# Kernel tuning notes

Hardware: AMD Instinct MI355X
Metric: run time of the kernel (lower is better)

## Reference

```python
import jax, jax.numpy as jnp
import numpy as np

H = 128
M = 50000
L = 400000
EPS = 1e-9


def setup_inputs() -> dict:
    key = jax.random.key(0)
    ks = jax.random.split(key, 24)
    d = {
        'x_emb': jax.random.normal(ks[0], (M, H), jnp.float32),
        'child_h': jax.random.normal(ks[1], (M, H), jnp.float32),
        'child_c': jax.random.normal(ks[2], (M, H), jnp.float32),
        'pair_cand_idx': jax.random.randint(ks[3], (L,), 0, M, jnp.int32),
        'pair_child_idx': jax.random.randint(ks[4], (L,), 0, M, jnp.int32),
    }
    s = 1.0 / np.sqrt(H)
    names = ['Wi_w', 'Ui_w', 'Wf_w', 'Uf_w', 'Wo_w', 'Uo_w', 'Wc_w', 'Uc_w', 'Wa_w', 'Ua_w']
    for i, n in enumerate(names):
        d[n] = jax.random.uniform(ks[5 + i], (H, H), jnp.float32, -s, s)
    for i, n in enumerate(['Wi_b', 'Wf_b', 'Wo_b', 'Wc_b', 'Wa_b']):
        d[n] = jax.random.uniform(ks[15 + i], (H,), jnp.float32, -s, s)
    d['v_w'] = jax.random.uniform(ks[20], (H,), jnp.float32, -s, s)
    return d


def reference(x_emb, child_h, child_c, pair_cand_idx, pair_child_idx,
              Wi_w, Ui_w, Wf_w, Uf_w, Wo_w, Uo_w, Wc_w, Uc_w, Wa_w, Ua_w,
              Wi_b, Wf_b, Wo_b, Wc_b, Wa_b, v_w):
    m = x_emb.shape[0]
    ci, chi = pair_cand_idx, pair_child_idx

    # --- segment attention (torch version runs under no_grad) ---
    Ah = child_h @ Wa_w.T + Wa_b          # [M,H]
    Bx = x_emb @ Ua_w.T                   # [M,H]
    e = jnp.tanh(Ah[chi] + Bx[ci]) @ v_w  # [L]
    seg_max = jax.ops.segment_max(e, ci, num_segments=m)
    x_exp = jnp.exp(e - seg_max[ci])
    seg_sum = jax.ops.segment_sum(x_exp, ci, num_segments=m) + EPS
    attn = x_exp / seg_sum[ci]            # [L]
    h_hat = jax.ops.segment_sum(attn[:, None] * child_h[chi], ci, num_segments=m)  # [M,H]

    # --- tree-LSTM gates ---
    i_j = jax.nn.sigmoid(x_emb @ Wi_w.T + Wi_b + h_hat @ Ui_w.T)
    Wfx = x_emb @ Wf_w.T + Wf_b
    Ufh = child_h @ Uf_w.T
    f_pair = jax.nn.sigmoid(Wfx[ci] + Ufh[chi])                       # [L,H]
    sum_f_c = jax.ops.segment_sum(f_pair * child_c[chi], ci, num_segments=m)
    c_t = jnp.tanh(x_emb @ Wc_w.T + Wc_b + h_hat @ Uc_w.T)
    c = i_j * c_t + sum_f_c
    o_j = jax.nn.sigmoid(x_emb @ Wo_w.T + Wo_b + h_hat @ Uo_w.T)
    h = o_j * jnp.tanh(c)
    return (h, c)
```

## Files before the change

kernel.cpp:

```cpp
#include <hip/hip_runtime.h>
#include <cstdint>
#include <cstddef>

#define H 128
#define PSTRIDE 512

typedef __bf16 v8bf __attribute__((ext_vector_type(8)));
typedef __bf16 v4bf __attribute__((ext_vector_type(4)));
typedef float  v4f  __attribute__((ext_vector_type(4)));

__device__ __forceinline__ float ftanh(float x) {
    return 1.f - 2.f / (1.f + __expf(2.f * x));
}
__device__ __forceinline__ float fsigm(float x) {
    return 1.f / (1.f + __expf(-x));
}

struct MatDesc {
    const __bf16* A;
    int           lda;
    const __bf16* Wb;
    const float*  bias;
    __bf16*       C;
    int           ldc;
};
struct MatBatch { MatDesc m[7]; };
struct WPtrs { const float* w[10]; };

__global__ __launch_bounds__(256) void prep_k(WPtrs wp, __bf16* __restrict__ Wb,
                                              const float* __restrict__ x,
                                              const float* __restrict__ chh,
                                              const float* __restrict__ chc,
                                              __bf16* __restrict__ xe,
                                              __bf16* __restrict__ P,
                                              const int* __restrict__ ci,
                                              int* __restrict__ counts,
                                              int MH4, int L) {
    int tid = blockIdx.x * 256 + threadIdx.x;
    if (tid < 40960) {
        int mat = tid >> 12;
        int off = (tid & 4095) << 2;
        v4f a = *(const v4f*)(wp.w[mat] + off);
        v4bf b;
#pragma unroll
        for (int k = 0; k < 4; ++k) b[k] = (__bf16)a[k];
        *(v4bf*)(Wb + mat * 16384 + off) = b;
        return;
    }
    int i = tid - 40960;
    if (i < MH4) {
        v4f a = ((const v4f*)x)[i];
        v4f b = ((const v4f*)chh)[i];
        v4f c = ((const v4f*)chc)[i];
        v4bf ab, bb, cb;
#pragma unroll
        for (int k = 0; k < 4; ++k) {
            ab[k] = (__bf16)a[k]; bb[k] = (__bf16)b[k]; cb[k] = (__bf16)c[k];
        }
        ((v4bf*)xe)[i] = ab;
        int m = i >> 5;
        int q = (i & 31) << 2;
        __bf16* prow = P + (size_t)m * PSTRIDE + q;
        *(v4bf*)prow = bb;
        *(v4bf*)(prow + H) = cb;
        return;
    }
    int l = i - MH4;
    if (l < L) atomicAdd(&counts[ci[l]], 1);
}

__global__ __launch_bounds__(256) void gemm_batch(MatBatch batch, int M, int ntile) {
    const int blk = blockIdx.x;
    const int g = blk / 56;
    const int w = blk % 56;
    const int j = w >> 3;
    const int t = (g << 3) | (w & 7);
    if (t >= ntile) return;
    const MatDesc d = batch.m[j];
    __shared__ __bf16 wlds[H][H + 8];

    for (int tt = threadIdx.x; tt < 2048; tt += 256) {
        int n = tt >> 4;
        int k = (tt & 15) << 3;
        *(v8bf*)&wlds[n][k] = *(const v8bf*)(d.Wb + n * H + k);
    }
    __syncthreads();

    const int wave = threadIdx.x >> 6;
    const int lane = threadIdx.x & 63;
    const int quad = lane >> 4;
    const int l16  = lane & 15;
    const int r0   = t * 128 + wave * 32;

    v4f acc0[8], acc1[8];
#pragma unroll
    for (int nt = 0; nt < 8; ++nt) {
        acc0[nt] = (v4f){0.f, 0.f, 0.f, 0.f};
        acc1[nt] = (v4f){0.f, 0.f, 0.f, 0.f};
    }

    const __bf16* ar0 = d.A + (size_t)(r0 + l16) * d.lda + quad * 8;
    const __bf16* ar1 = d.A + (size_t)(r0 + 16 + l16) * d.lda + quad * 8;
#pragma unroll
    for (int k0 = 0; k0 < H; k0 += 32) {
        v8bf a0 = *(const v8bf*)(ar0 + k0);
        v8bf a1 = *(const v8bf*)(ar1 + k0);
#pragma unroll
        for (int nt = 0; nt < 8; ++nt) {
            v8bf b = *(const v8bf*)(&wlds[nt * 16 + l16][k0 + quad * 8]);
            acc0[nt] = __builtin_amdgcn_mfma_f32_16x16x32_bf16(a0, b, acc0[nt], 0, 0, 0);
            acc1[nt] = __builtin_amdgcn_mfma_f32_16x16x32_bf16(a1, b, acc1[nt], 0, 0, 0);
        }
    }

#pragma unroll
    for (int nt = 0; nt < 8; ++nt) {
        int n = nt * 16 + l16;
        float bia = d.bias ? d.bias[n] : 0.f;
#pragma unroll
        for (int r = 0; r < 4; ++r) {
            int m0 = r0 + quad * 4 + r;
            int m1 = m0 + 16;
            if (m0 < M) d.C[(size_t)m0 * d.ldc + n] = (__bf16)(acc0[nt][r] + bia);
            if (m1 < M) d.C[(size_t)m1 * d.ldc + n] = (__bf16)(acc1[nt][r] + bia);
        }
    }
}

__global__ __launch_bounds__(256) void edge_scatter(const int* __restrict__ ci,
                                                    const int* __restrict__ chi,
                                                    const float* __restrict__ vw,
                                                    const __bf16* __restrict__ Bx,
                                                    const __bf16* __restrict__ P,
                                                    int* __restrict__ cursor,
                                                    int* __restrict__ payload,
                                                    float* __restrict__ exs, int L) {
    int e = blockIdx.x * 8 + (threadIdx.x >> 5);
    if (e >= L) return;
    const int l32 = threadIdx.x & 31;
    const int h = l32 << 2;
    int m  = ci[e];
    int cj = chi[e];

    v4bf a4 = *(const v4bf*)(P + (cj << 9) + 3 * H + h);
    v4bf b4 = *(const v4bf*)(Bx + (m << 7) + h);
    v4f  vv = *(const v4f*)(vw + h);

    float s = 0.f;
#pragma unroll
    for (int k = 0; k < 4; ++k) s += ftanh((float)a4[k] + (float)b4[k]) * vv[k];
    s += __shfl_xor(s, 1);
    s += __shfl_xor(s, 2);
    s += __shfl_xor(s, 4);
    s += __shfl_xor(s, 8);
    s += __shfl_xor(s, 16);
    if (l32 == 0) {
        int pos = atomicAdd(&cursor[m], 1);
        payload[pos] = cj;
        exs[pos] = __expf(s);
    }
}

__global__ __launch_bounds__(1024) void scan_local(const int* __restrict__ counts,
                                                   int* __restrict__ excl,
                                                   int* __restrict__ bsums, int M) {
    __shared__ int s[1024];
    int tid = threadIdx.x;
    int idx = blockIdx.x * 1024 + tid;
    int v = (idx < M) ? counts[idx] : 0;
    s[tid] = v;
    __syncthreads();
    for (int off = 1; off < 1024; off <<= 1) {
        int t = (tid >= off) ? s[tid - off] : 0;
        __syncthreads();
        s[tid] += t;
        __syncthreads();
    }
    if (idx < M) excl[idx] = s[tid] - v;
    if (tid == 1023) bsums[blockIdx.x] = s[1023];
}

__global__ __launch_bounds__(1024) void scan_fused(int* __restrict__ rowptr,
                                                   int* __restrict__ cursor,
                                                   const int* __restrict__ bsums,
                                                   const int* __restrict__ counts,
                                                   int M, int nb) {
    __shared__ int s[1024];
    int t = threadIdx.x, b = blockIdx.x;
    int v = (t < nb) ? bsums[t] : 0;
    s[t] = v;
    __syncthreads();
    for (int off = 1; off < 1024; off <<= 1) {
        int tt = (t >= off) ? s[t - off] : 0;
        __syncthreads();
        s[t] += tt;
        __syncthreads();
    }
    int boff = (b == 0) ? 0 : s[b - 1];
    int idx = b * 1024 + t;
    if (idx < M) {
        int val = rowptr[idx] + boff;
        rowptr[idx] = val;
        cursor[idx] = val;
        if (idx == M - 1) rowptr[M] = val + counts[M - 1];
    }
}

__global__ __launch_bounds__(256) void segment_fused(const int* __restrict__ rowptr,
                                                     const int* __restrict__ payload,
                                                     const float* __restrict__ exs,
                                                     const __bf16* __restrict__ Wfx,
                                                     const __bf16* __restrict__ P,
                                                     __bf16* __restrict__ hhat,
                                                     float* __restrict__ sumfc, int M) {
    const int wl   = threadIdx.x & 63;
    const int half = wl & 32;
    const int l32  = wl & 31;
    const int m = blockIdx.x * 8 + (threadIdx.x >> 5);
    if (m >= M) return;
    const int start = rowptr[m];
    const int deg   = rowptr[m + 1] - start;
    const int h = l32 << 2;

    v4bf wf4 = *(const v4bf*)(Wfx + (m << 7) + h);
    float wff[4];
#pragma unroll
    for (int k = 0; k < 4; ++k) wff[k] = (float)wf4[k];

    int   pl0 = (l32 < deg) ? payload[start + l32] : 0;
    int   pl1 = (32 + l32 < deg) ? payload[start + 32 + l32] : 0;
    float ex0 = (l32 < deg) ? exs[start + l32] : 0.f;
    float ex1 = (32 + l32 < deg) ? exs[start + 32 + l32] : 0.f;

    float denom = 0.f;
    float acch[4] = {0.f, 0.f, 0.f, 0.f};
    float accf[4] = {0.f, 0.f, 0.f, 0.f};

    const int jcap = deg < 64 ? deg : 64;
    for (int j = 0; j < jcap; ++j) {
        int   cj = __shfl((j & 32) ? pl1 : pl0, half | (j & 31), 64);
        float ex = __shfl((j & 32) ? ex1 : ex0, half | (j & 31), 64);
        int off = (cj << 9) + h;
        v4bf h4 = *(const v4bf*)(P + off);
        v4bf c4 = *(const v4bf*)(P + off + H);
        v4bf u4 = *(const v4bf*)(P + off + 2 * H);
        denom += ex;
#pragma unroll
        for (int k = 0; k < 4; ++k) {
            acch[k] = fmaf(ex, (float)h4[k], acch[k]);
            accf[k] += fsigm(wff[k] + (float)u4[k]) * (float)c4[k];
        }
    }
    for (int j = 64; j < deg; ++j) {
        int   cj = payload[start + j];
        float ex = exs[start + j];
        int off = (cj << 9) + h;
        v4bf h4 = *(const v4bf*)(P + off);
        v4bf c4 = *(const v4bf*)(P + off + H);
        v4bf u4 = *(const v4bf*)(P + off + 2 * H);
        denom += ex;
#pragma unroll
        for (int k = 0; k < 4; ++k) {
            acch[k] = fmaf(ex, (float)h4[k], acch[k]);
            accf[k] += fsigm(wff[k] + (float)u4[k]) * (float)c4[k];
        }
    }

    float inv = 1.f / (denom + 1e-9f);
    v4bf hb;
    v4f sf;
#pragma unroll
    for (int k = 0; k < 4; ++k) { hb[k] = (__bf16)(acch[k] * inv); sf[k] = accf[k]; }
    *(v4bf*)(hhat + (size_t)m * H + h) = hb;
    *(v4f*)(sumfc + (size_t)m * H + h) = sf;
}

__global__ __launch_bounds__(256) void gemm_final(const __bf16* __restrict__ hhat,
                                                  const __bf16* __restrict__ Ui,
                                                  const __bf16* __restrict__ Uc,
                                                  const __bf16* __restrict__ Uo,
                                                  const __bf16* __restrict__ Xi,
                                                  const __bf16* __restrict__ Xc,
                                                  const __bf16* __restrict__ Xo,
                                                  const float* __restrict__ sumfc,
                                                  float* __restrict__ out, int M, int MH) {
    const int wave = threadIdx.x >> 6;
    const int lane = threadIdx.x & 63;
    const int quad = lane >> 4;
    const int l16  = lane & 15;
    const int r0   = blockIdx.x * 128 + wave * 32;

    const __bf16* p0 = hhat + (size_t)(r0 + l16) * H + quad * 8;
    const __bf16* p1 = hhat + (size_t)(r0 + 16 + l16) * H + quad * 8;
    v8bf a0[4], a1[4];
#pragma unroll
    for (int k0 = 0; k0 < 4; ++k0) {
        a0[k0] = *(const v8bf*)(p0 + k0 * 32);
        a1[k0] = *(const v8bf*)(p1 + k0 * 32);
    }

#pragma unroll
    for (int nt = 0; nt < 8; ++nt) {
        const int boff = (nt * 16 + l16) * H + quad * 8;
        v4f ai0 = (v4f){0.f, 0.f, 0.f, 0.f}, ai1 = ai0;
        v4f ac0 = ai0, ac1 = ai0, ao0 = ai0, ao1 = ai0;
#pragma unroll
        for (int k0 = 0; k0 < 4; ++k0) {
            v8bf bi = *(const v8bf*)(Ui + boff + k0 * 32);
            v8bf bc = *(const v8bf*)(Uc + boff + k0 * 32);
            v8bf bo = *(const v8bf*)(Uo + boff + k0 * 32);
            ai0 = __builtin_amdgcn_mfma_f32_16x16x32_bf16(a0[k0], bi, ai0, 0, 0, 0);
            ai1 = __builtin_amdgcn_mfma_f32_16x16x32_bf16(a1[k0], bi, ai1, 0, 0, 0);
            ac0 = __builtin_amdgcn_mfma_f32_16x16x32_bf16(a0[k0], bc, ac0, 0, 0, 0);
            ac1 = __builtin_amdgcn_mfma_f32_16x16x32_bf16(a1[k0], bc, ac1, 0, 0, 0);
            ao0 = __builtin_amdgcn_mfma_f32_16x16x32_bf16(a0[k0], bo, ao0, 0, 0, 0);
            ao1 = __builtin_amdgcn_mfma_f32_16x16x32_bf16(a1[k0], bo, ao1, 0, 0, 0);
        }
        int n = nt * 16 + l16;
#pragma unroll
        for (int r = 0; r < 4; ++r) {
            int m0 = r0 + quad * 4 + r;
            if (m0 < M) {
                size_t idx = (size_t)m0 * H + n;
                float ig = fsigm((float)Xi[idx] + ai0[r]);
                float ct = ftanh((float)Xc[idx] + ac0[r]);
                float og = fsigm((float)Xo[idx] + ao0[r]);
                float c = ig * ct + sumfc[idx];
                out[idx] = og * ftanh(c);
                out[MH + idx] = c;
            }
            int m1 = m0 + 16;
            if (m1 < M) {
                size_t idx = (size_t)m1 * H + n;
                float ig = fsigm((float)Xi[idx] + ai1[r]);
                float ct = ftanh((float)Xc[idx] + ac1[r]);
                float og = fsigm((float)Xo[idx] + ao1[r]);
                float c = ig * ct + sumfc[idx];
                out[idx] = og * ftanh(c);
                out[MH + idx] = c;
            }
        }
    }
}

extern "C" void kernel_launch(void* const* d_in, const int* in_sizes, int n_in,
                              void* d_out, int out_size, void* d_ws, size_t ws_size,
                              hipStream_t stream) {
    const float* x_emb   = (const float*)d_in[0];
    const float* child_h = (const float*)d_in[1];
    const float* child_c = (const float*)d_in[2];
    const int*   ci      = (const int*)d_in[3];
    const int*   chi     = (const int*)d_in[4];
    const float* Wi_b = (const float*)d_in[15];
    const float* Wf_b = (const float*)d_in[16];
    const float* Wo_b = (const float*)d_in[17];
    const float* Wc_b = (const float*)d_in[18];
    const float* Wa_b = (const float*)d_in[19];
    const float* vw   = (const float*)d_in[20];

    const int M    = in_sizes[0] / H;
    const int L    = in_sizes[3];
    const int Mpad = (M + 127) & ~127;
    const int MH   = M * H;
    const int MH4  = MH / 4;

    char* p = (char*)d_ws;
    auto alloc = [&](size_t bytes) {
        char* r = p;
        p += (bytes + 255) & ~(size_t)255;
        return (void*)r;
    };
    size_t bfbytes = (size_t)Mpad * H * sizeof(__bf16);
    __bf16* xe16   = (__bf16*)alloc(bfbytes);
    __bf16* P      = (__bf16*)alloc((size_t)Mpad * PSTRIDE * sizeof(__bf16));
    __bf16* hhat16 = (__bf16*)alloc(bfbytes);
    __bf16* Bx16   = (__bf16*)alloc(bfbytes);
    __bf16* Wfx16  = (__bf16*)alloc(bfbytes);
    __bf16* Xi16   = (__bf16*)alloc(bfbytes);
    __bf16* Xc16   = (__bf16*)alloc(bfbytes);
    __bf16* Xo16   = (__bf16*)alloc(bfbytes);
    __bf16* Wb     = (__bf16*)alloc(10 * 16384 * sizeof(__bf16));
    float* sumfc   = (float*)alloc((size_t)MH * 4);
    float* exs     = (float*)alloc((size_t)L * 4);
    int*   payload = (int*)alloc((size_t)L * 4);
    int*   counts  = (int*)alloc((size_t)M * 4);
    int*   rowptr  = (int*)alloc((size_t)(M + 1) * 4);
    int*   cursor  = (int*)alloc((size_t)M * 4);
    int*   bsums   = (int*)alloc(1024 * 4);

    hipMemsetAsync(counts, 0, (size_t)M * 4, stream);

    WPtrs wp;
    for (int k = 0; k < 10; ++k) wp.w[k] = (const float*)d_in[5 + k];
    int prep_items = 40960 + MH4 + L;
    prep_k<<<(prep_items + 255) / 256, 256, 0, stream>>>(wp, Wb, x_emb, child_h, child_c,
                                                         xe16, P, ci, counts, MH4, L);

    const __bf16* Wi = Wb + 0 * 16384;
    const __bf16* Ui = Wb + 1 * 16384;
    const __bf16* Wf = Wb + 2 * 16384;
    const __bf16* Uf = Wb + 3 * 16384;
    const __bf16* Wo = Wb + 4 * 16384;
    const __bf16* Uo = Wb + 5 * 16384;
    const __bf16* Wc = Wb + 6 * 16384;
    const __bf16* Uc = Wb + 7 * 16384;
    const __bf16* Wa = Wb + 8 * 16384;
    const __bf16* Ua = Wb + 9 * 16384;

    MatBatch ba{};
    ba.m[0] = MatDesc{P,    PSTRIDE, Wa, Wa_b,    P + 3 * H, PSTRIDE};
    ba.m[1] = MatDesc{xe16, H,       Ua, nullptr, Bx16,      H};
    ba.m[2] = MatDesc{xe16, H,       Wf, Wf_b,    Wfx16,     H};
    ba.m[3] = MatDesc{P,    PSTRIDE, Uf, nullptr, P + 2 * H, PSTRIDE};
    ba.m[4] = MatDesc{xe16, H,       Wi, Wi_b,    Xi16,      H};
    ba.m[5] = MatDesc{xe16, H,       Wc, Wc_b,    Xc16,      H};
    ba.m[6] = MatDesc{xe16, H,       Wo, Wo_b,    Xo16,      H};
    const int ntile = Mpad / 128;
    const int ntile8 = (ntile + 7) & ~7;
    gemm_batch<<<7 * ntile8, 256, 0, stream>>>(ba, M, ntile);

    int nb = (M + 1023) / 1024;
    scan_local<<<nb, 1024, 0, stream>>>(counts, rowptr, bsums, M);
    scan_fused<<<nb, 1024, 0, stream>>>(rowptr, cursor, bsums, counts, M, nb);

    edge_scatter<<<(L + 7) / 8, 256, 0, stream>>>(ci, chi, vw, Bx16, P, cursor,
                                                  payload, exs, L);

    segment_fused<<<(M + 7) / 8, 256, 0, stream>>>(rowptr, payload, exs, Wfx16, P,
                                                   hhat16, sumfc, M);

    gemm_final<<<Mpad / 128, 256, 0, stream>>>(hhat16, Ui, Uc, Uo, Xi16, Xc16, Xo16,
                                               sumfc, (float*)d_out, M, MH);
}
```

Before: 412.6 us.

## Fuse attention score computation into segment kernel and read fp32 x_emb directly in GEMM

The per-edge attention score (tanh dot product and exp) moves out of the edge scatter kernel into the per-segment reduction kernel. The scatter becomes a thin one-thread-per-edge CSR fill, and the exs buffer is no longer written or read. The batched GEMM now converts fp32 x_emb to bf16 on the fly, so the separate bf16 copy of x_emb in prep is dropped. The segment loop is unrolled by two to overlap gathers; the cost is an extra 128-element gather per edge in the segment kernel and five x_emb GEMMs each reading fp32 inputs.

Result: slower. 428.4 us (+3.8%).

```diff
diff --git a/kernel.cpp b/kernel.cpp
--- a/kernel.cpp
+++ b/kernel.cpp
@@ -17,8 +17,9 @@
 }
 
 struct MatDesc {
-    const __bf16* A;
+    const void*   A;
     int           lda;
+    int           af32;
     const __bf16* Wb;
     const float*  bias;
     __bf16*       C;
@@ -28,10 +29,8 @@
 struct WPtrs { const float* w[10]; };
 
 __global__ __launch_bounds__(256) void prep_k(WPtrs wp, __bf16* __restrict__ Wb,
-                                              const float* __restrict__ x,
                                               const float* __restrict__ chh,
                                               const float* __restrict__ chc,
-                                              __bf16* __restrict__ xe,
                                               __bf16* __restrict__ P,
                                               const int* __restrict__ ci,
                                               int* __restrict__ counts,
@@ -49,15 +48,11 @@
     }
     int i = tid - 40960;
     if (i < MH4) {
-        v4f a = ((const v4f*)x)[i];
         v4f b = ((const v4f*)chh)[i];
         v4f c = ((const v4f*)chc)[i];
-        v4bf ab, bb, cb;
-#pragma unroll
-        for (int k = 0; k < 4; ++k) {
-            ab[k] = (__bf16)a[k]; bb[k] = (__bf16)b[k]; cb[k] = (__bf16)c[k];
-        }
-        ((v4bf*)xe)[i] = ab;
+        v4bf bb, cb;
+#pragma unroll
+        for (int k = 0; k < 4; ++k) { bb[k] = (__bf16)b[k]; cb[k] = (__bf16)c[k]; }
         int m = i >> 5;
         int q = (i & 31) << 2;
         __bf16* prow = P + (size_t)m * PSTRIDE + q;
@@ -92,6 +87,39 @@
     const int l16  = lane & 15;
     const int r0   = t * 128 + wave * 32;
 
+    int ra = r0 + l16;      if (ra > M - 1) ra = M - 1;
+    int rb = r0 + 16 + l16; if (rb > M - 1) rb = M - 1;
+
+    v8bf a0[4], a1[4];
+    if (d.af32) {
+        const float* A = (const float*)d.A;
+        const float* p0 = A + (size_t)ra * d.lda + quad * 8;
+        const float* p1 = A + (size_t)rb * d.lda + quad * 8;
+#pragma unroll
+        for (int k0 = 0; k0 < 4; ++k0) {
+            v4f x0a = *(const v4f*)(p0 + k0 * 32);
+            v4f x0b = *(const v4f*)(p0 + k0 * 32 + 4);
+            v4f x1a = *(const v4f*)(p1 + k0 * 32);
+            v4f x1b = *(const v4f*)(p1 + k0 * 32 + 4);
+            v8bf t0, t1;
+#pragma unroll
+            for (int k = 0; k < 4; ++k) {
+                t0[k] = (__bf16)x0a[k]; t0[k + 4] = (__bf16)x0b[k];
+                t1[k] = (__bf16)x1a[k]; t1[k + 4] = (__bf16)x1b[k];
+            }
+            a0[k0] = t0; a1[k0] = t1;
+        }
+    } else {
+        const __bf16* A = (const __bf16*)d.A;
+        const __bf16* p0 = A + (size_t)ra * d.lda + quad * 8;
+        const __bf16* p1 = A + (size_t)rb * d.lda + quad * 8;
+#pragma unroll
+        for (int k0 = 0; k0 < 4; ++k0) {
+            a0[k0] = *(const v8bf*)(p0 + k0 * 32);
+            a1[k0] = *(const v8bf*)(p1 + k0 * 32);
+        }
+    }
+
     v4f acc0[8], acc1[8];
 #pragma unroll
     for (int nt = 0; nt < 8; ++nt) {
@@ -99,17 +127,13 @@
         acc1[nt] = (v4f){0.f, 0.f, 0.f, 0.f};
     }
 
-    const __bf16* ar0 = d.A + (size_t)(r0 + l16) * d.lda + quad * 8;
-    const __bf16* ar1 = d.A + (size_t)(r0 + 16 + l16) * d.lda + quad * 8;
-#pragma unroll
-    for (int k0 = 0; k0 < H; k0 += 32) {
-        v8bf a0 = *(const v8bf*)(ar0 + k0);
-        v8bf a1 = *(const v8bf*)(ar1 + k0);
+#pragma unroll
+    for (int k0 = 0; k0 < 4; ++k0) {
 #pragma unroll
         for (int nt = 0; nt < 8; ++nt) {
-            v8bf b = *(const v8bf*)(&wlds[nt * 16 + l16][k0 + quad * 8]);
-            acc0[nt] = __builtin_amdgcn_mfma_f32_16x16x32_bf16(a0, b, acc0[nt], 0, 0, 0);
-            acc1[nt] = __builtin_amdgcn_mfma_f32_16x16x32_bf16(a1, b, acc1[nt], 0, 0, 0);
+            v8bf b = *(const v8bf*)(&wlds[nt * 16 + l16][k0 * 32 + quad * 8]);
+            acc0[nt] = __builtin_amdgcn_mfma_f32_16x16x32_bf16(a0[k0], b, acc0[nt], 0, 0, 0);
+            acc1[nt] = __builtin_amdgcn_mfma_f32_16x16x32_bf16(a1[k0], b, acc1[nt], 0, 0, 0);
         }
     }
 
@@ -124,40 +148,6 @@
             if (m0 < M) d.C[(size_t)m0 * d.ldc + n] = (__bf16)(acc0[nt][r] + bia);
             if (m1 < M) d.C[(size_t)m1 * d.ldc + n] = (__bf16)(acc1[nt][r] + bia);
         }
-    }
-}
-
-__global__ __launch_bounds__(256) void edge_scatter(const int* __restrict__ ci,
-                                                    const int* __restrict__ chi,
-                                                    const float* __restrict__ vw,
-                                                    const __bf16* __restrict__ Bx,
-                                                    const __bf16* __restrict__ P,
-                                                    int* __restrict__ cursor,
-                                                    int* __restrict__ payload,
-                                                    float* __restrict__ exs, int L) {
-    int e = blockIdx.x * 8 + (threadIdx.x >> 5);
-    if (e >= L) return;
-    const int l32 = threadIdx.x & 31;
-    const int h = l32 << 2;
-    int m  = ci[e];
-    int cj = chi[e];
-
-    v4bf a4 = *(const v4bf*)(P + (cj << 9) + 3 * H + h);
-    v4bf b4 = *(const v4bf*)(Bx + (m << 7) + h);
-    v4f  vv = *(const v4f*)(vw + h);
-
-    float s = 0.f;
-#pragma unroll
-    for (int k = 0; k < 4; ++k) s += ftanh((float)a4[k] + (float)b4[k]) * vv[k];
-    s += __shfl_xor(s, 1);
-    s += __shfl_xor(s, 2);
-    s += __shfl_xor(s, 4);
-    s += __shfl_xor(s, 8);
-    s += __shfl_xor(s, 16);
-    if (l32 == 0) {
-        int pos = atomicAdd(&cursor[m], 1);
-        payload[pos] = cj;
-        exs[pos] = __expf(s);
     }
 }
 
@@ -206,9 +196,21 @@
     }
 }
 
+__global__ __launch_bounds__(256) void scatter_k(const int* __restrict__ ci,
+                                                 const int* __restrict__ chi,
+                                                 int* __restrict__ cursor,
+                                                 int* __restrict__ payload, int L) {
+    int l = blockIdx.x * 256 + threadIdx.x;
+    if (l < L) {
+        int pos = atomicAdd(&cursor[ci[l]], 1);
+        payload[pos] = chi[l];
+    }
+}
+
 __global__ __launch_bounds__(256) void segment_fused(const int* __restrict__ rowptr,
                                                      const int* __restrict__ payload,
-                                                     const float* __restrict__ exs,
+                                                     const float* __restrict__ vw,
+                                                     const __bf16* __restrict__ Bx,
                                                      const __bf16* __restrict__ Wfx,
                                                      const __bf16* __restrict__ P,
                                                      __bf16* __restrict__ hhat,
@@ -222,28 +224,73 @@
     const int deg   = rowptr[m + 1] - start;
     const int h = l32 << 2;
 
+    v4bf bx4 = *(const v4bf*)(Bx + (m << 7) + h);
     v4bf wf4 = *(const v4bf*)(Wfx + (m << 7) + h);
-    float wff[4];
-#pragma unroll
-    for (int k = 0; k < 4; ++k) wff[k] = (float)wf4[k];
-
-    int   pl0 = (l32 < deg) ? payload[start + l32] : 0;
-    int   pl1 = (32 + l32 < deg) ? payload[start + 32 + l32] : 0;
-    float ex0 = (l32 < deg) ? exs[start + l32] : 0.f;
-    float ex1 = (32 + l32 < deg) ? exs[start + 32 + l32] : 0.f;
+    v4f  vv  = *(const v4f*)(vw + h);
+    float bxf[4], wff[4];
+#pragma unroll
+    for (int k = 0; k < 4; ++k) { bxf[k] = (float)bx4[k]; wff[k] = (float)wf4[k]; }
+
+    int pl0 = (l32 < deg) ? payload[start + l32] : 0;
+    int pl1 = (32 + l32 < deg) ? payload[start + 32 + l32] : 0;
 
     float denom = 0.f;
     float acch[4] = {0.f, 0.f, 0.f, 0.f};
     float accf[4] = {0.f, 0.f, 0.f, 0.f};
 
     const int jcap = deg < 64 ? deg : 64;
-    for (int j = 0; j < jcap; ++j) {
-        int   cj = __shfl((j & 32) ? pl1 : pl0, half | (j & 31), 64);
-        float ex = __shfl((j & 32) ? ex1 : ex0, half | (j & 31), 64);
-        int off = (cj << 9) + h;
-        v4bf h4 = *(const v4bf*)(P + off);
-        v4bf c4 = *(const v4bf*)(P + off + H);
-        v4bf u4 = *(const v4bf*)(P + off + 2 * H);
+    int j = 0;
+    for (; j + 2 <= jcap; j += 2) {
+        int cj0 = __shfl((j & 32) ? pl1 : pl0, half | (j & 31), 64);
+        int cj1 = __shfl((j & 32) ? pl1 : pl0, half | ((j + 1) & 31), 64);
+        const __bf16* pb0 = P + ((size_t)cj0 << 9) + h;
+        const __bf16* pb1 = P + ((size_t)cj1 << 9) + h;
+        v4bf h40 = *(const v4bf*)pb0;
+        v4bf c40 = *(const v4bf*)(pb0 + H);
+        v4bf u40 = *(const v4bf*)(pb0 + 2 * H);
+        v4bf a40 = *(const v4bf*)(pb0 + 3 * H);
+        v4bf h41 = *(const v4bf*)pb1;
+        v4bf c41 = *(const v4bf*)(pb1 + H);
+        v4bf u41 = *(const v4bf*)(pb1 + 2 * H);
+        v4bf a41 = *(const v4bf*)(pb1 + 3 * H);
+        float s0 = 0.f, s1 = 0.f;
+#pragma unroll
+        for (int k = 0; k < 4; ++k) {
+            s0 += ftanh((float)a40[k] + bxf[k]) * vv[k];
+            s1 += ftanh((float)a41[k] + bxf[k]) * vv[k];
+        }
+        s0 += __shfl_xor(s0, 1);  s1 += __shfl_xor(s1, 1);
+        s0 += __shfl_xor(s0, 2);  s1 += __shfl_xor(s1, 2);
+        s0 += __shfl_xor(s0, 4);  s1 += __shfl_xor(s1, 4);
+        s0 += __shfl_xor(s0, 8);  s1 += __shfl_xor(s1, 8);
+        s0 += __shfl_xor(s0, 16); s1 += __shfl_xor(s1, 16);
+        float ex0 = __expf(s0);
+        float ex1 = __expf(s1);
+        denom += ex0 + ex1;
+#pragma unroll
+        for (int k = 0; k < 4; ++k) {
+            acch[k] = fmaf(ex0, (float)h40[k], acch[k]);
+            acch[k] = fmaf(ex1, (float)h41[k], acch[k]);
+            accf[k] += fsigm(wff[k] + (float)u40[k]) * (float)c40[k];
+            accf[k] += fsigm(wff[k] + (float)u41[k]) * (float)c41[k];
+        }
+    }
+    for (; j < jcap; ++j) {
+        int cj = __shfl((j & 32) ? pl1 : pl0, half | (j & 31), 64);
+        const __bf16* pb = P + ((size_t)cj << 9) + h;
+        v4bf h4 = *(const v4bf*)pb;
+        v4bf c4 = *(const v4bf*)(pb + H);
+        v4bf u4 = *(const v4bf*)(pb + 2 * H);
+        v4bf a4 = *(const v4bf*)(pb + 3 * H);
+        float s = 0.f;
+#pragma unroll
+        for (int k = 0; k < 4; ++k) s += ftanh((float)a4[k] + bxf[k]) * vv[k];
+        s += __shfl_xor(s, 1);
+        s += __shfl_xor(s, 2);
+        s += __shfl_xor(s, 4);
+        s += __shfl_xor(s, 8);
+        s += __shfl_xor(s, 16);
+        float ex = __expf(s);
         denom += ex;
 #pragma unroll
         for (int k = 0; k < 4; ++k) {
@@ -251,13 +298,22 @@
             accf[k] += fsigm(wff[k] + (float)u4[k]) * (float)c4[k];
         }
     }
-    for (int j = 64; j < deg; ++j) {
-        int   cj = payload[start + j];
-        float ex = exs[start + j];
-        int off = (cj << 9) + h;
-        v4bf h4 = *(const v4bf*)(P + off);
-        v4bf c4 = *(const v4bf*)(P + off + H);
-        v4bf u4 = *(const v4bf*)(P + off + 2 * H);
+    for (int jj = 64; jj < deg; ++jj) {
+        int cj = payload[start + jj];
+        const __bf16* pb = P + ((size_t)cj << 9) + h;
+        v4bf h4 = *(const v4bf*)pb;
+        v4bf c4 = *(const v4bf*)(pb + H);
+        v4bf u4 = *(const v4bf*)(pb + 2 * H);
+        v4bf a4 = *(const v4bf*)(pb + 3 * H);
+        float s = 0.f;
+#pragma unroll
+        for (int k = 0; k < 4; ++k) s += ftanh((float)a4[k] + bxf[k]) * vv[k];
+        s += __shfl_xor(s, 1);
+        s += __shfl_xor(s, 2);
+        s += __shfl_xor(s, 4);
+        s += __shfl_xor(s, 8);
+        s += __shfl_xor(s, 16);
+        float ex = __expf(s);
         denom += ex;
 #pragma unroll
         for (int k = 0; k < 4; ++k) {
@@ -371,7 +427,6 @@
         return (void*)r;
     };
     size_t bfbytes = (size_t)Mpad * H * sizeof(__bf16);
-    __bf16* xe16   = (__bf16*)alloc(bfbytes);
     __bf16* P      = (__bf16*)alloc((size_t)Mpad * PSTRIDE * sizeof(__bf16));
     __bf16* hhat16 = (__bf16*)alloc(bfbytes);
     __bf16* Bx16   = (__bf16*)alloc(bfbytes);
@@ -381,7 +436,6 @@
     __bf16* Xo16   = (__bf16*)alloc(bfbytes);
     __bf16* Wb     = (__bf16*)alloc(10 * 16384 * sizeof(__bf16));
     float* sumfc   = (float*)alloc((size_t)MH * 4);
-    float* exs     = (float*)alloc((size_t)L * 4);
     int*   payload = (int*)alloc((size_t)L * 4);
     int*   counts  = (int*)alloc((size_t)M * 4);
     int*   rowptr  = (int*)alloc((size_t)(M + 1) * 4);
@@ -393,8 +447,8 @@
     WPtrs wp;
     for (int k = 0; k < 10; ++k) wp.w[k] = (const float*)d_in[5 + k];
     int prep_items = 40960 + MH4 + L;
-    prep_k<<<(prep_items + 255) / 256, 256, 0, stream>>>(wp, Wb, x_emb, child_h, child_c,
-                                                         xe16, P, ci, counts, MH4, L);
+    prep_k<<<(prep_items + 255) / 256, 256, 0, stream>>>(wp, Wb, child_h, child_c,
+                                                         P, ci, counts, MH4, L);
 
     const __bf16* Wi = Wb + 0 * 16384;
     const __bf16* Ui = Wb + 1 * 16384;
@@ -408,13 +462,13 @@
     const __bf16* Ua = Wb + 9 * 16384;
 
     MatBatch ba{};
-    ba.m[0] = MatDesc{P,    PSTRIDE, Wa, Wa_b,    P + 3 * H, PSTRIDE};
-    ba.m[1] = MatDesc{xe16, H,       Ua, nullptr, Bx16,      H};
-    ba.m[2] = MatDesc{xe16, H,       Wf, Wf_b,    Wfx16,     H};
-    ba.m[3] = MatDesc{P,    PSTRIDE, Uf, nullptr, P + 2 * H, PSTRIDE};
-    ba.m[4] = MatDesc{xe16, H,       Wi, Wi_b,    Xi16,      H};
-    ba.m[5] = MatDesc{xe16, H,       Wc, Wc_b,    Xc16,      H};
-    ba.m[6] = MatDesc{xe16, H,       Wo, Wo_b,    Xo16,      H};
+    ba.m[0] = MatDesc{P,     PSTRIDE, 0, Wa, Wa_b,    P + 3 * H, PSTRIDE};
+    ba.m[1] = MatDesc{x_emb, H,       1, Ua, nullptr, Bx16,      H};
+    ba.m[2] = MatDesc{x_emb, H,       1, Wf, Wf_b,    Wfx16,     H};
+    ba.m[3] = MatDesc{P,     PSTRIDE, 0, Uf, nullptr, P + 2 * H, PSTRIDE};
+    ba.m[4] = MatDesc{x_emb, H,       1, Wi, Wi_b,    Xi16,      H};
+    ba.m[5] = MatDesc{x_emb, H,       1, Wc, Wc_b,    Xc16,      H};
+    ba.m[6] = MatDesc{x_emb, H,       1, Wo, Wo_b,    Xo16,      H};
     const int ntile = Mpad / 128;
     const int ntile8 = (ntile + 7) & ~7;
     gemm_batch<<<7 * ntile8, 256, 0, stream>>>(ba, M, ntile);
@@ -423,10 +477,9 @@
     scan_local<<<nb, 1024, 0, stream>>>(counts, rowptr, bsums, M);
     scan_fused<<<nb, 1024, 0, stream>>>(rowptr, cursor, bsums, counts, M, nb);
 
-    edge_scatter<<<(L + 7) / 8, 256, 0, stream>>>(ci, chi, vw, Bx16, P, cursor,
-                                                  payload, exs, L);
-
-    segment_fused<<<(M + 7) / 8, 256, 0, stream>>>(rowptr, payload, exs, Wfx16, P,
+    scatter_k<<<(L + 255) / 256, 256, 0, stream>>>(ci, chi, cursor, payload, L);
+
+    segment_fused<<<(M + 7) / 8, 256, 0, stream>>>(rowptr, payload, vw, Bx16, Wfx16, P,
                                                    hhat16, sumfc, M);
 
     gemm_final<<<Mpad / 128, 256, 0, stream>>>(hhat16, Ui, Uc, Uo, Xi16, Xc16, Xo16,
```

## Fuse attention score into segment kernel and interleave per-child row layout

Applied to the files above, without the earlier changes.

The per-edge attention score computation moves out of the separate edge_scatter kernel and into segment_fused, so scores are computed on the fly during the segment pass. This removes the exs buffer and the extra gather of child rows. The P row layout is interleaved into 16-element chunks (h, c, Uf, Ah per 4 columns), so each lane fetches all four operands with two 16-byte loads instead of four 8-byte loads. The GEMM now reads A from a compact child_h bf16 copy, preloads all A fragments with clamped rows, and writes to P through a strided scatter. The DPP/swizzle reduction replaces shuffles, and block size drops to 128.

Result: no change. 412.4 us (-0.0%).

```diff
diff --git a/kernel.cpp b/kernel.cpp
--- a/kernel.cpp
+++ b/kernel.cpp
@@ -14,6 +14,20 @@
 }
 __device__ __forceinline__ float fsigm(float x) {
     return 1.f / (1.f + __expf(-x));
+}
+
+__device__ __forceinline__ float red32(float s) {
+    int x;
+    x = __builtin_amdgcn_update_dpp(0, __float_as_int(s), 0xB1, 0xF, 0xF, true);
+    s += __int_as_float(x);
+    x = __builtin_amdgcn_update_dpp(0, __float_as_int(s), 0x4E, 0xF, 0xF, true);
+    s += __int_as_float(x);
+    x = __builtin_amdgcn_update_dpp(0, __float_as_int(s), 0x141, 0xF, 0xF, true);
+    s += __int_as_float(x);
+    x = __builtin_amdgcn_update_dpp(0, __float_as_int(s), 0x140, 0xF, 0xF, true);
+    s += __int_as_float(x);
+    x = __builtin_amdgcn_ds_swizzle(__float_as_int(s), 0x401F);
+    return s + __int_as_float(x);
 }
 
 struct MatDesc {
@@ -23,6 +37,7 @@
     const float*  bias;
     __bf16*       C;
     int           ldc;
+    int           psec;
 };
 struct MatBatch { MatDesc m[7]; };
 struct WPtrs { const float* w[10]; };
@@ -32,6 +47,7 @@
                                               const float* __restrict__ chh,
                                               const float* __restrict__ chc,
                                               __bf16* __restrict__ xe,
+                                              __bf16* __restrict__ chA,
                                               __bf16* __restrict__ P,
                                               const int* __restrict__ ci,
                                               int* __restrict__ counts,
@@ -58,11 +74,12 @@
             ab[k] = (__bf16)a[k]; bb[k] = (__bf16)b[k]; cb[k] = (__bf16)c[k];
         }
         ((v4bf*)xe)[i] = ab;
+        ((v4bf*)chA)[i] = bb;
         int m = i >> 5;
-        int q = (i & 31) << 2;
-        __bf16* prow = P + (size_t)m * PSTRIDE + q;
+        int q = i & 31;
+        __bf16* prow = P + (size_t)m * PSTRIDE + (q << 4);
         *(v4bf*)prow = bb;
-        *(v4bf*)(prow + H) = cb;
+        *(v4bf*)(prow + 4) = cb;
         return;
     }
     int l = i - MH4;
@@ -92,6 +109,18 @@
     const int l16  = lane & 15;
     const int r0   = t * 128 + wave * 32;
 
+    int ra = r0 + l16;      if (ra > M - 1) ra = M - 1;
+    int rb = r0 + 16 + l16; if (rb > M - 1) rb = M - 1;
+
+    const __bf16* p0 = d.A + (size_t)ra * d.lda + quad * 8;
+    const __bf16* p1 = d.A + (size_t)rb * d.lda + quad * 8;
+    v8bf a0[4], a1[4];
+#pragma unroll
+    for (int k0 = 0; k0 < 4; ++k0) {
+        a0[k0] = *(const v8bf*)(p0 + k0 * 32);
+        a1[k0] = *(const v8bf*)(p1 + k0 * 32);
+    }
+
     v4f acc0[8], acc1[8];
 #pragma unroll
     for (int nt = 0; nt < 8; ++nt) {
@@ -99,65 +128,44 @@
         acc1[nt] = (v4f){0.f, 0.f, 0.f, 0.f};
     }
 
-    const __bf16* ar0 = d.A + (size_t)(r0 + l16) * d.lda + quad * 8;
-    const __bf16* ar1 = d.A + (size_t)(r0 + 16 + l16) * d.lda + quad * 8;
-#pragma unroll
-    for (int k0 = 0; k0 < H; k0 += 32) {
-        v8bf a0 = *(const v8bf*)(ar0 + k0);
-        v8bf a1 = *(const v8bf*)(ar1 + k0);
+#pragma unroll
+    for (int k0 = 0; k0 < 4; ++k0) {
 #pragma unroll
         for (int nt = 0; nt < 8; ++nt) {
-            v8bf b = *(const v8bf*)(&wlds[nt * 16 + l16][k0 + quad * 8]);
-            acc0[nt] = __builtin_amdgcn_mfma_f32_16x16x32_bf16(a0, b, acc0[nt], 0, 0, 0);
-            acc1[nt] = __builtin_amdgcn_mfma_f32_16x16x32_bf16(a1, b, acc1[nt], 0, 0, 0);
-        }
-    }
-
-#pragma unroll
-    for (int nt = 0; nt < 8; ++nt) {
-        int n = nt * 16 + l16;
-        float bia = d.bias ? d.bias[n] : 0.f;
-#pragma unroll
-        for (int r = 0; r < 4; ++r) {
-            int m0 = r0 + quad * 4 + r;
-            int m1 = m0 + 16;
-            if (m0 < M) d.C[(size_t)m0 * d.ldc + n] = (__bf16)(acc0[nt][r] + bia);
-            if (m1 < M) d.C[(size_t)m1 * d.ldc + n] = (__bf16)(acc1[nt][r] + bia);
-        }
-    }
-}
-
-__global__ __launch_bounds__(256) void edge_scatter(const int* __restrict__ ci,
-                                                    const int* __restrict__ chi,
-                                                    const float* __restrict__ vw,
-                                                    const __bf16* __restrict__ Bx,
-                                                    const __bf16* __restrict__ P,
-                                                    int* __restrict__ cursor,
-                                                    int* __restrict__ payload,
-                                                    float* __restrict__ exs, int L) {
-    int e = blockIdx.x * 8 + (threadIdx.x >> 5);
-    if (e >= L) return;
-    const int l32 = threadIdx.x & 31;
-    const int h = l32 << 2;
-    int m  = ci[e];
-    int cj = chi[e];
-
-    v4bf a4 = *(const v4bf*)(P + (cj << 9) + 3 * H + h);
-    v4bf b4 = *(const v4bf*)(Bx + (m << 7) + h);
-    v4f  vv = *(const v4f*)(vw + h);
-
-    float s = 0.f;
-#pragma unroll
-    for (int k = 0; k < 4; ++k) s += ftanh((float)a4[k] + (float)b4[k]) * vv[k];
-    s += __shfl_xor(s, 1);
-    s += __shfl_xor(s, 2);
-    s += __shfl_xor(s, 4);
-    s += __shfl_xor(s, 8);
-    s += __shfl_xor(s, 16);
-    if (l32 == 0) {
-        int pos = atomicAdd(&cursor[m], 1);
-        payload[pos] = cj;
-        exs[pos] = __expf(s);
+            v8bf b = *(const v8bf*)(&wlds[nt * 16 + l16][k0 * 32 + quad * 8]);
+            acc0[nt] = __builtin_amdgcn_mfma_f32_16x16x32_bf16(a0[k0], b, acc0[nt], 0, 0, 0);
+            acc1[nt] = __builtin_amdgcn_mfma_f32_16x16x32_bf16(a1[k0], b, acc1[nt], 0, 0, 0);
+        }
+    }
+
+    if (d.psec >= 0) {
+        const int so = d.psec << 2;
+#pragma unroll
+        for (int nt = 0; nt < 8; ++nt) {
+            int n = nt * 16 + l16;
+            float bia = d.bias ? d.bias[n] : 0.f;
+            size_t col = ((size_t)(n >> 2) << 4) + so + (n & 3);
+#pragma unroll
+            for (int r = 0; r < 4; ++r) {
+                int m0 = r0 + quad * 4 + r;
+                int m1 = m0 + 16;
+                if (m0 < M) d.C[(size_t)m0 * PSTRIDE + col] = (__bf16)(acc0[nt][r] + bia);
+                if (m1 < M) d.C[(size_t)m1 * PSTRIDE + col] = (__bf16)(acc1[nt][r] + bia);
+            }
+        }
+    } else {
+#pragma unroll
+        for (int nt = 0; nt < 8; ++nt) {
+            int n = nt * 16 + l16;
+            float bia = d.bias ? d.bias[n] : 0.f;
+#pragma unroll
+            for (int r = 0; r < 4; ++r) {
+                int m0 = r0 + quad * 4 + r;
+                int m1 = m0 + 16;
+                if (m0 < M) d.C[(size_t)m0 * d.ldc + n] = (__bf16)(acc0[nt][r] + bia);
+                if (m1 < M) d.C[(size_t)m1 * d.ldc + n] = (__bf16)(acc1[nt][r] + bia);
+            }
+        }
     }
 }
 
@@ -206,9 +214,21 @@
     }
 }
 
-__global__ __launch_bounds__(256) void segment_fused(const int* __restrict__ rowptr,
+__global__ __launch_bounds__(256) void scatter_k(const int* __restrict__ ci,
+                                                 const int* __restrict__ chi,
+                                                 int* __restrict__ cursor,
+                                                 int* __restrict__ payload, int L) {
+    int l = blockIdx.x * 256 + threadIdx.x;
+    if (l < L) {
+        int pos = atomicAdd(&cursor[ci[l]], 1);
+        payload[pos] = chi[l];
+    }
+}
+
+__global__ __launch_bounds__(128) void segment_fused(const int* __restrict__ rowptr,
                                                      const int* __restrict__ payload,
-                                                     const float* __restrict__ exs,
+                                                     const float* __restrict__ vw,
+                                                     const __bf16* __restrict__ Bx,
                                                      const __bf16* __restrict__ Wfx,
                                                      const __bf16* __restrict__ P,
                                                      __bf16* __restrict__ hhat,
@@ -216,21 +236,22 @@
     const int wl   = threadIdx.x & 63;
     const int half = wl & 32;
     const int l32  = wl & 31;
-    const int m = blockIdx.x * 8 + (threadIdx.x >> 5);
+    const int m = blockIdx.x * 4 + (threadIdx.x >> 5);
     if (m >= M) return;
     const int start = rowptr[m];
     const int deg   = rowptr[m + 1] - start;
-    const int h = l32 << 2;
-
+    const int h   = l32 << 2;
+    const int q16 = l32 << 4;
+
+    v4bf bx4 = *(const v4bf*)(Bx + (m << 7) + h);
     v4bf wf4 = *(const v4bf*)(Wfx + (m << 7) + h);
-    float wff[4];
-#pragma unroll
-    for (int k = 0; k < 4; ++k) wff[k] = (float)wf4[k];
-
-    int   pl0 = (l32 < deg) ? payload[start + l32] : 0;
-    int   pl1 = (32 + l32 < deg) ? payload[start + 32 + l32] : 0;
-    float ex0 = (l32 < deg) ? exs[start + l32] : 0.f;
-    float ex1 = (32 + l32 < deg) ? exs[start + 32 + l32] : 0.f;
+    v4f  vv  = *(const v4f*)(vw + h);
+    float bxf[4], wff[4];
+#pragma unroll
+    for (int k = 0; k < 4; ++k) { bxf[k] = (float)bx4[k]; wff[k] = (float)wf4[k]; }
+
+    int pl0 = (l32 < deg) ? payload[start + l32] : 0;
+    int pl1 = (32 + l32 < deg) ? payload[start + 32 + l32] : 0;
 
     float denom = 0.f;
     float acch[4] = {0.f, 0.f, 0.f, 0.f};
@@ -238,31 +259,37 @@
 
     const int jcap = deg < 64 ? deg : 64;
     for (int j = 0; j < jcap; ++j) {
-        int   cj = __shfl((j & 32) ? pl1 : pl0, half | (j & 31), 64);
-        float ex = __shfl((j & 32) ? ex1 : ex0, half | (j & 31), 64);
-        int off = (cj << 9) + h;
-        v4bf h4 = *(const v4bf*)(P + off);
-        v4bf c4 = *(const v4bf*)(P + off + H);
-        v4bf u4 = *(const v4bf*)(P + off + 2 * H);
+        int cj = __shfl((j & 32) ? pl1 : pl0, half | (j & 31), 64);
+        const __bf16* pb = P + ((size_t)cj << 9) + q16;
+        v8bf x0 = *(const v8bf*)pb;
+        v8bf x1 = *(const v8bf*)(pb + 8);
+        float s = 0.f;
+#pragma unroll
+        for (int k = 0; k < 4; ++k) s += ftanh((float)x1[4 + k] + bxf[k]) * vv[k];
+        s = red32(s);
+        float ex = __expf(s);
         denom += ex;
 #pragma unroll
         for (int k = 0; k < 4; ++k) {
-            acch[k] = fmaf(ex, (float)h4[k], acch[k]);
-            accf[k] += fsigm(wff[k] + (float)u4[k]) * (float)c4[k];
+            acch[k] = fmaf(ex, (float)x0[k], acch[k]);
+            accf[k] += fsigm(wff[k] + (float)x1[k]) * (float)x0[4 + k];
         }
     }
     for (int j = 64; j < deg; ++j) {
-        int   cj = payload[start + j];
-        float ex = exs[start + j];
-        int off = (cj << 9) + h;
-        v4bf h4 = *(const v4bf*)(P + off);
-        v4bf c4 = *(const v4bf*)(P + off + H);
-        v4bf u4 = *(const v4bf*)(P + off + 2 * H);
+        int cj = payload[start + j];
+        const __bf16* pb = P + ((size_t)cj << 9) + q16;
+        v8bf x0 = *(const v8bf*)pb;
+        v8bf x1 = *(const v8bf*)(pb + 8);
+        float s = 0.f;
+#pragma unroll
+        for (int k = 0; k < 4; ++k) s += ftanh((float)x1[4 + k] + bxf[k]) * vv[k];
+        s = red32(s);
+        float ex = __expf(s);
         denom += ex;
 #pragma unroll
         for (int k = 0; k < 4; ++k) {
-            acch[k] = fmaf(ex, (float)h4[k], acch[k]);
-            accf[k] += fsigm(wff[k] + (float)u4[k]) * (float)c4[k];
+            acch[k] = fmaf(ex, (float)x0[k], acch[k]);
+            accf[k] += fsigm(wff[k] + (float)x1[k]) * (float)x0[4 + k];
         }
     }
 
@@ -372,6 +399,7 @@
     };
     size_t bfbytes = (size_t)Mpad * H * sizeof(__bf16);
     __bf16* xe16   = (__bf16*)alloc(bfbytes);
+    __bf16* chA16  = (__bf16*)alloc(bfbytes);
     __bf16* P      = (__bf16*)alloc((size_t)Mpad * PSTRIDE * sizeof(__bf16));
     __bf16* hhat16 = (__bf16*)alloc(bfbytes);
     __bf16* Bx16   = (__bf16*)alloc(bfbytes);
@@ -381,7 +409,6 @@
     __bf16* Xo16   = (__bf16*)alloc(bfbytes);
     __bf16* Wb     = (__bf16*)alloc(10 * 16384 * sizeof(__bf16));
     float* sumfc   = (float*)alloc((size_t)MH * 4);
-    float* exs     = (float*)alloc((size_t)L * 4);
     int*   payload = (int*)alloc((size_t)L * 4);
     int*   counts  = (int*)alloc((size_t)M * 4);
     int*   rowptr  = (int*)alloc((size_t)(M + 1) * 4);
@@ -394,7 +421,7 @@
     for (int k = 0; k < 10; ++k) wp.w[k] = (const float*)d_in[5 + k];
     int prep_items = 40960 + MH4 + L;
     prep_k<<<(prep_items + 255) / 256, 256, 0, stream>>>(wp, Wb, x_emb, child_h, child_c,
-                                                         xe16, P, ci, counts, MH4, L);
+                                                         xe16, chA16, P, ci, counts, MH4, L);
 
     const __bf16* Wi = Wb + 0 * 16384;
     const __bf16* Ui = Wb + 1 * 16384;
@@ -408,13 +435,13 @@
     const __bf16* Ua = Wb + 9 * 16384;
 
     MatBatch ba{};
-    ba.m[0] = MatDesc{P,    PSTRIDE, Wa, Wa_b,    P + 3 * H, PSTRIDE};
-    ba.m[1] = MatDesc{xe16, H,       Ua, nullptr, Bx16,      H};
-    ba.m[2] = MatDesc{xe16, H,       Wf, Wf_b,    Wfx16,     H};
-    ba.m[3] = MatDesc{P,    PSTRIDE, Uf, nullptr, P + 2 * H, PSTRIDE};
-    ba.m[4] = MatDesc{xe16, H,       Wi, Wi_b,    Xi16,      H};
-    ba.m[5] = MatDesc{xe16, H,       Wc, Wc_b,    Xc16,      H};
-    ba.m[6] = MatDesc{xe16, H,       Wo, Wo_b,    Xo16,      H};
+    ba.m[0] = MatDesc{chA16, H, Wa, Wa_b,    P,     0, 3};
+    ba.m[1] = MatDesc{xe16,  H, Ua, nullptr, Bx16,  H, -1};
+    ba.m[2] = MatDesc{xe16,  H, Wf, Wf_b,    Wfx16, H, -1};
+    ba.m[3] = MatDesc{chA16, H, Uf, nullptr, P,     0, 2};
+    ba.m[4] = MatDesc{xe16,  H, Wi, Wi_b,    Xi16,  H, -1};
+    ba.m[5] = MatDesc{xe16,  H, Wc, Wc_b,    Xc16,  H, -1};
+    ba.m[6] = MatDesc{xe16,  H, Wo, Wo_b,    Xo16,  H, -1};
     const int ntile = Mpad / 128;
     const int ntile8 = (ntile + 7) & ~7;
     gemm_batch<<<7 * ntile8, 256, 0, stream>>>(ba, M, ntile);
@@ -423,10 +450,9 @@
     scan_local<<<nb, 1024, 0, stream>>>(counts, rowptr, bsums, M);
     scan_fused<<<nb, 1024, 0, stream>>>(rowptr, cursor, bsums, counts, M, nb);
 
-    edge_scatter<<<(L + 7) / 8, 256, 0, stream>>>(ci, chi, vw, Bx16, P, cursor,
-                                                  payload, exs, L);
-
-    segment_fused<<<(M + 7) / 8, 256, 0, stream>>>(rowptr, payload, exs, Wfx16, P,
+    scatter_k<<<(L + 255) / 256, 256, 0, stream>>>(ci, chi, cursor, payload, L);
+
+    segment_fused<<<(M + 3) / 4, 128, 0, stream>>>(rowptr, payload, vw, Bx16, Wfx16, P,
                                                    hhat16, sumfc, M);
 
     gemm_final<<<Mpad / 128, 256, 0, stream>>>(hhat16, Ui, Uc, Uo, Xi16, Xc16, Xo16,
```
